# Kernel tuning notes

Hardware: AMD Instinct MI355X
Metric: run time of the kernel (lower is better)

Reference implementation:

```python
import jax, jax.numpy as jnp
import numpy as np

KERNEL, STRIDE = 3, 2
IN_DIM, OUT_DIM = 32, 32
POSE = 4
POSE_LEN = POSE * POSE
ITERS = 3
LAM = 0.01
EPS = 1e-8


def setup_inputs() -> dict:
    key = jax.random.key(0)
    k1, k2, k3, k4 = jax.random.split(key, 4)
    B, H, W = 8, 24, 24
    capsules = jax.random.uniform(k1, (B, H, W, IN_DIM, POSE_LEN + 1), dtype=jnp.float32)
    trans_mat = jax.random.normal(k2, (KERNEL, KERNEL, IN_DIM, OUT_DIM, POSE, POSE), dtype=jnp.float32)
    beta_u = jax.random.normal(k3, (1,), dtype=jnp.float32)
    beta_a = jax.random.normal(k4, (1,), dtype=jnp.float32)
    return {"capsules": capsules, "trans_mat": trans_mat, "beta_u": beta_u, "beta_a": beta_a}


def _extract_patches(capsules, h, w):
    # capsules: [B,H,W,Ci,F] -> [B,h*w,k,k,Ci,F] (strided kernel x kernel windows)
    rows = STRIDE * jnp.arange(h)[:, None] + jnp.arange(KERNEL)[None, :]  # [h,k]
    cols = STRIDE * jnp.arange(w)[:, None] + jnp.arange(KERNEL)[None, :]  # [w,k]
    p = capsules[:, rows]                # [B,h,k,W,Ci,F]
    p = p[:, :, :, cols]                 # [B,h,k,w,k,Ci,F]
    p = jnp.transpose(p, (0, 1, 3, 2, 4, 5, 6))  # [B,h,w,k,k,Ci,F]
    B = capsules.shape[0]
    return p.reshape(B, h * w, KERNEL, KERNEL, IN_DIM, p.shape[-1])


def _em_routing(V, a, beta_u, beta_a):
    # V: [B,N,I,O,P] votes, a: [B,N,I,1,1] input activations
    B, N, I, O, P = V.shape
    R = jnp.full((B, N, I, O, 1), 1.0 / O, dtype=V.dtype)
    mu = a_out = None
    for it in range(ITERS):
        # ---- M-step: weighted Gaussian statistics per output capsule ----
        Ra = R * a                                            # [B,N,I,O,1]
        sum_R = Ra.sum(axis=2, keepdims=True) + EPS           # [B,N,1,O,1]
        mu = (Ra * V).sum(axis=2, keepdims=True) / sum_R      # [B,N,1,O,P]
        sigma_sq = (Ra * (V - mu) ** 2).sum(axis=2, keepdims=True) / sum_R + EPS
        cost = (beta_u + 0.5 * jnp.log(sigma_sq)) * sum_R     # [B,N,1,O,P]
        a_out = jax.nn.sigmoid(LAM * (beta_a - cost.sum(axis=-1, keepdims=True)))  # [B,N,1,O,1]
        if it < ITERS - 1:
            # ---- E-step: posterior assignment R via Gaussian log-pdf ----
            ln_p = (-((V - mu) ** 2) / (2.0 * sigma_sq)
                    - 0.5 * jnp.log(2.0 * jnp.pi * sigma_sq)).sum(axis=-1, keepdims=True)  # [B,N,I,O,1]
            R = jax.nn.softmax(ln_p + jnp.log(a_out + EPS), axis=3)
    return mu[:, :, 0], a_out[:, :, 0, :, 0]  # [B,N,O,P], [B,N,O]


def reference(capsules, trans_mat, beta_u, beta_a):
    B, H, W = capsules.shape[:3]
    h = (H - KERNEL + 1) // STRIDE
    w = (W - KERNEL + 1) // STRIDE
    patches = _extract_patches(capsules, h, w)  # [B,N,k,k,Ci,P^2+1]
    poses = patches[..., :-1].reshape(B, h * w, KERNEL, KERNEL, IN_DIM, POSE, POSE)
    acts = patches[..., -1]                      # [B,N,k,k,Ci]
    # votes: per-(k,k,Ci,Co) pose-matrix product, vectorized over all patches
    votes = jnp.einsum('bnxyipq,xyioqr->bnxyiopr', poses, trans_mat)
    V = votes.reshape(B, h * w, KERNEL * KERNEL * IN_DIM, OUT_DIM, POSE_LEN)
    a = acts.reshape(B, h * w, KERNEL * KERNEL * IN_DIM, 1, 1)
    mu, a_out = _em_routing(V, a, beta_u, beta_a)
    out = jnp.concatenate([mu.reshape(B, h, w, OUT_DIM, POSE_LEN),
                           a_out.reshape(B, h, w, OUT_DIM, 1)], axis=-1)
    return out  # [B,h,w,out_dim,pose_len+1]
```

## Files before the change

### kernel.cpp

```cpp
#include <hip/hip_runtime.h>
#include <math.h>


namespace {

constexpr int NH   = 11;
constexpr int NI   = 288;
constexpr float LAM_   = 0.01f;
constexpr float EPS_   = 1e-8f;
constexpr float LOG2PI = 1.8378770664093453f;

typedef __attribute__((ext_vector_type(2))) float f32x2;

__device__ __forceinline__ f32x2 splat(float s) { return (f32x2){s, s}; }
__device__ __forceinline__ f32x2 vfma(f32x2 a, f32x2 b, f32x2 c) {
    return __builtin_elementwise_fma(a, b, c);
}

__device__ __forceinline__ float red32_max(float x) {
    int y;
    y = __builtin_amdgcn_update_dpp(0, __float_as_int(x), 0xB1, 0xF, 0xF, true);
    x = fmaxf(x, __int_as_float(y));
    y = __builtin_amdgcn_update_dpp(0, __float_as_int(x), 0x4E, 0xF, 0xF, true);
    x = fmaxf(x, __int_as_float(y));
    y = __builtin_amdgcn_update_dpp(0, __float_as_int(x), 0x141, 0xF, 0xF, true);
    x = fmaxf(x, __int_as_float(y));
    y = __builtin_amdgcn_update_dpp(0, __float_as_int(x), 0x140, 0xF, 0xF, true);
    x = fmaxf(x, __int_as_float(y));
    y = __builtin_amdgcn_ds_swizzle(__float_as_int(x), 0x401F);
    x = fmaxf(x, __int_as_float(y));
    return x;
}
__device__ __forceinline__ float red32_sum(float x) {
    int y;
    y = __builtin_amdgcn_update_dpp(0, __float_as_int(x), 0xB1, 0xF, 0xF, true);
    x += __int_as_float(y);
    y = __builtin_amdgcn_update_dpp(0, __float_as_int(x), 0x4E, 0xF, 0xF, true);
    x += __int_as_float(y);
    y = __builtin_amdgcn_update_dpp(0, __float_as_int(x), 0x141, 0xF, 0xF, true);
    x += __int_as_float(y);
    y = __builtin_amdgcn_update_dpp(0, __float_as_int(x), 0x140, 0xF, 0xF, true);
    x += __int_as_float(y);
    y = __builtin_amdgcn_ds_swizzle(__float_as_int(x), 0x401F);
    x += __int_as_float(y);
    return x;
}

__device__ __forceinline__ void votes_pk(const float4* __restrict__ Prow4,
                                         const f32x2 T2[4][2], f32x2 V2[4][2]) {
    float4 pr0 = Prow4[0], pr1 = Prow4[1], pr2 = Prow4[2], pr3 = Prow4[3];
#pragma unroll
    for (int h = 0; h < 2; ++h) {
        {
            f32x2 s = splat(pr0.x) * T2[0][h];
            s = vfma(splat(pr0.y), T2[1][h], s);
            s = vfma(splat(pr0.z), T2[2][h], s);
            V2[0][h] = vfma(splat(pr0.w), T2[3][h], s);
        }
        {
            f32x2 s = splat(pr1.x) * T2[0][h];
            s = vfma(splat(pr1.y), T2[1][h], s);
            s = vfma(splat(pr1.z), T2[2][h], s);
            V2[1][h] = vfma(splat(pr1.w), T2[3][h], s);
        }
        {
            f32x2 s = splat(pr2.x) * T2[0][h];
            s = vfma(splat(pr2.y), T2[1][h], s);
            s = vfma(splat(pr2.z), T2[2][h], s);
            V2[2][h] = vfma(splat(pr2.w), T2[3][h], s);
        }
        {
            f32x2 s = splat(pr3.x) * T2[0][h];
            s = vfma(splat(pr3.y), T2[1][h], s);
            s = vfma(splat(pr3.z), T2[2][h], s);
            V2[3][h] = vfma(splat(pr3.w), T2[3][h], s);
        }
    }
}

__device__ __forceinline__ void load_T2(const float4* __restrict__ tp, f32x2 T2[4][2]) {
    float4 b0 = tp[0], b1 = tp[1], b2 = tp[2], b3 = tp[3];
    T2[0][0] = (f32x2){b0.x, b0.y};  T2[0][1] = (f32x2){b0.z, b0.w};
    T2[1][0] = (f32x2){b1.x, b1.y};  T2[1][1] = (f32x2){b1.z, b1.w};
    T2[2][0] = (f32x2){b2.x, b2.y};  T2[2][1] = (f32x2){b2.z, b2.w};
    T2[3][0] = (f32x2){b3.x, b3.y};  T2[3][1] = (f32x2){b3.z, b3.w};
}

template<int BASE>
__device__ __forceinline__ float finalize_half(const f32x2* m1v, const f32x2* m2v,
        const float* __restrict__ r0, const float* __restrict__ r1,
        const float* __restrict__ r2, float S, float rs, bool last,
        float* __restrict__ mu_dst, float* __restrict__ i2s_dst)
{
    float csum = 0.f;
#pragma unroll
    for (int p = 0; p < 8; ++p) {
        constexpr int B = BASE;
        float m1k = m1v[(B + p) >> 1][(B + p) & 1];
        float m2k = m2v[(B + p) >> 1][(B + p) & 1];
        float M1f = m1k + r0[B + p] + r1[B + p] + r2[B + p];
        float M2f = m2k + r0[16 + B + p] + r1[16 + B + p] + r2[16 + B + p];
        float m  = M1f * rs;
        float sg = (M2f - 2.f * m * M1f + m * m * S) * rs + EPS_;
        csum += __logf(sg);
        mu_dst[B + p] = m;
        if (!last) i2s_dst[B + p] = __fdividef(0.5f, sg);
    }
    return csum;
}

__global__ __launch_bounds__(256, 4)
void convcaps_em_kernel(const float* __restrict__ caps,
                        const float* __restrict__ Tm,
                        const float* __restrict__ bu_p,
                        const float* __restrict__ ba_p,
                        float* __restrict__ out)
{
    __shared__ float pose_s[NI][16];
    __shared__ float act_s[NI];
    __shared__ float red_s[3][32][33];
    __shared__ float mu_s[32][18];
    __shared__ float i2s_s[32][18];
    __shared__ float C_s[32];
    __shared__ float fin_s[32][17];

    const int n  = blockIdx.x;
    const int b  = blockIdx.y;
    const int oy = n / NH;
    const int ox = n - oy * NH;
    const int t  = (int)threadIdx.x;
    const int o  = t & 31;
    const int ig = t >> 5;
    const int wv = t >> 6;
    const int ln = t & 63;
    const int hi = ln >> 5;

    for (int idx = t; idx < 9 * 544; idx += 256) {
        int cell = idx / 544;
        int j    = idx - cell * 544;
        int kx   = cell / 3;
        int ky   = cell - kx * 3;
        size_t src = ((((size_t)b * 24 + (2 * oy + kx)) * 24 + (2 * ox + ky)) * 32) * 17 + j;
        float v = caps[src];
        int ic = j / 17;
        int c  = j - ic * 17;
        int i  = cell * 32 + ic;
        if (c == 16) act_s[i] = v;
        else         pose_s[i][c] = v;
    }
    __syncthreads();

    const float beta_u = bu_p[0];
    const float beta_a = ba_p[0];
    const size_t oblk = ((((size_t)b * NH + oy) * NH + ox) * 32) * 17;

    f32x2 m1v[8], m2v[8];
    float sR;

#pragma unroll
    for (int j = 0; j < 8; ++j) { m1v[j] = splat(0.f); m2v[j] = splat(0.f); }
    sR = 0.f;
    {
        const float4* tptr = reinterpret_cast<const float4*>(Tm) + ((size_t)ig * 32 + o) * 4;
        for (int ii = 0; ii < NI / 8; ++ii, tptr += 1024) {
            const int i = ig + ii * 8;
            float ra = act_s[i] * (1.0f / 32.0f);
            f32x2 T2[4][2], V2[4][2];
            load_T2(tptr, T2);
            votes_pk(reinterpret_cast<const float4*>(&pose_s[i][0]), T2, V2);
            f32x2 ra2 = splat(ra);
#pragma unroll
            for (int p = 0; p < 4; ++p) {
#pragma unroll
                for (int h = 0; h < 2; ++h) {
                    f32x2 rv = ra2 * V2[p][h];
                    m1v[p * 2 + h] += rv;
                    m2v[p * 2 + h] = vfma(rv, V2[p][h], m2v[p * 2 + h]);
                }
            }
            sR += ra;
        }
    }

    for (int it = 0; it < 3; ++it) {
#pragma unroll
        for (int j = 0; j < 8; ++j) {
            m1v[j][0] += __shfl_xor(m1v[j][0], 32);
            m1v[j][1] += __shfl_xor(m1v[j][1], 32);
            m2v[j][0] += __shfl_xor(m2v[j][0], 32);
            m2v[j][1] += __shfl_xor(m2v[j][1], 32);
        }
        sR += __shfl_xor(sR, 32);
        if (wv > 0 && ln < 32) {
#pragma unroll
            for (int j = 0; j < 8; ++j) {
                red_s[wv - 1][o][2 * j]          = m1v[j][0];
                red_s[wv - 1][o][2 * j + 1]      = m1v[j][1];
                red_s[wv - 1][o][16 + 2 * j]     = m2v[j][0];
                red_s[wv - 1][o][16 + 2 * j + 1] = m2v[j][1];
            }
            red_s[wv - 1][o][32] = sR;
        }
        __syncthreads();

        if (wv == 0) {
            const bool last = (it == 2);
            const float* r0 = &red_s[0][o][0];
            const float* r1 = &red_s[1][o][0];
            const float* r2 = &red_s[2][o][0];
            float S    = sR + r0[32] + r1[32] + r2[32];
            float sumR = S + EPS_;
            float rs   = __fdividef(1.f, sumR);
            float* mu_dst  = last ? &fin_s[o][0] : &mu_s[o][0];
            float* i2s_dst = &i2s_s[o][0];
            float csum = (hi == 0)
                ? finalize_half<0>(m1v, m2v, r0, r1, r2, S, rs, last, mu_dst, i2s_dst)
                : finalize_half<8>(m1v, m2v, r0, r1, r2, S, rs, last, mu_dst, i2s_dst);
            csum *= 0.5f;
            float L = csum + __shfl_xor(csum, 32);
            float cost = sumR * (16.f * beta_u + L);
            float a = __fdividef(1.f, 1.f + __expf(-(LAM_ * (beta_a - cost))));
            if (hi == 0) {
                if (last) fin_s[o][16] = a;
                else      C_s[o] = __logf(a + EPS_) - (L + 8.f * LOG2PI);
            }
        }
        if (it == 2) break;
        __syncthreads();

        const float Cc = C_s[o];
        f32x2 MU2[8], IS2[8];
        {
            const f32x2* mrow = reinterpret_cast<const f32x2*>(&mu_s[o][0]);
            const f32x2* irow = reinterpret_cast<const f32x2*>(&i2s_s[o][0]);
#pragma unroll
            for (int j = 0; j < 8; ++j) { MU2[j] = mrow[j]; IS2[j] = irow[j]; }
        }

#pragma unroll
        for (int j = 0; j < 8; ++j) { m1v[j] = splat(0.f); m2v[j] = splat(0.f); }
        sR = 0.f;

        const float4* tptr = reinterpret_cast<const float4*>(Tm) + ((size_t)ig * 32 + o) * 4;
        for (int ii = 0; ii < NI / 8; ++ii, tptr += 1024) {
            const int i = ig + ii * 8;
            f32x2 T2[4][2], V2[4][2];
            load_T2(tptr, T2);
            votes_pk(reinterpret_cast<const float4*>(&pose_s[i][0]), T2, V2);

            f32x2 q2 = splat(0.f);
#pragma unroll
            for (int p = 0; p < 4; ++p) {
#pragma unroll
                for (int h = 0; h < 2; ++h) {
                    f32x2 d = V2[p][h] - MU2[p * 2 + h];
                    q2 = vfma(d * d, IS2[p * 2 + h], q2);
                }
            }
            float lnp = Cc - (q2[0] + q2[1]);

            float mx = red32_max(lnp);
            float e  = __expf(lnp - mx);
            float sm = red32_sum(e);
            float ra = __fdividef(act_s[i] * e, sm);

            f32x2 ra2 = splat(ra);
#pragma unroll
            for (int p = 0; p < 4; ++p) {
#pragma unroll
                for (int h = 0; h < 2; ++h) {
                    f32x2 rv = ra2 * V2[p][h];
                    m1v[p * 2 + h] += rv;
                    m2v[p * 2 + h] = vfma(rv, V2[p][h], m2v[p * 2 + h]);
                }
            }
            sR += ra;
        }
    }

    __syncthreads();
    for (int k = t; k < 544; k += 256) {
        out[oblk + k] = (&fin_s[0][0])[k];
    }
}

}

extern "C" void kernel_launch(void* const* d_in, const int* in_sizes, int n_in,
                              void* d_out, int out_size, void* d_ws, size_t ws_size,
                              hipStream_t stream) {
    const float* caps = (const float*)d_in[0];
    const float* Tm   = (const float*)d_in[1];
    const float* bu   = (const float*)d_in[2];
    const float* ba   = (const float*)d_in[3];
    float* out        = (float*)d_out;

    dim3 grid(121, 8);
    dim3 block(256);
    hipLaunchKernelGGL(convcaps_em_kernel, grid, block, 0, stream,
                       caps, Tm, bu, ba, out);
}
```

Baseline: 135.5 us.

## Software-pipeline E-step accumulation and drop per-input max reduction in softmax

The E-step loop is restructured so each step computes votes and the routing exponent for input i while accumulating the M-step statistics of input i-1 with double-buffered vote registers. This hides the cross-lane sum-reduction latency behind independent FMAs. The per-input max reduction is replaced by a single max of the per-output constant, which is a valid upper bound because the quadratic term is non-negative. Log-domain constants are pre-scaled by log2(e) so exp2f can be used, and the kernel is pinned to 4 waves per EU. The looser softmax shift risks underflow when the quadratic terms are large.

```diff
diff --git a/kernel.cpp b/kernel.cpp
--- a/kernel.cpp
+++ b/kernel.cpp
@@ -9,6 +9,7 @@
 constexpr float LAM_   = 0.01f;
 constexpr float EPS_   = 1e-8f;
 constexpr float LOG2PI = 1.8378770664093453f;
+constexpr float LOG2E  = 1.4426950408889634f;
 
 typedef __attribute__((ext_vector_type(2))) float f32x2;
 
@@ -46,44 +47,44 @@
     return x;
 }
 
+__device__ __forceinline__ void load_T2(const float4* __restrict__ tp, f32x2 T2[8]) {
+    float4 b0 = tp[0], b1 = tp[1], b2 = tp[2], b3 = tp[3];
+    T2[0] = (f32x2){b0.x, b0.y};  T2[1] = (f32x2){b0.z, b0.w};
+    T2[2] = (f32x2){b1.x, b1.y};  T2[3] = (f32x2){b1.z, b1.w};
+    T2[4] = (f32x2){b2.x, b2.y};  T2[5] = (f32x2){b2.z, b2.w};
+    T2[6] = (f32x2){b3.x, b3.y};  T2[7] = (f32x2){b3.z, b3.w};
+}
+
 __device__ __forceinline__ void votes_pk(const float4* __restrict__ Prow4,
-                                         const f32x2 T2[4][2], f32x2 V2[4][2]) {
+                                         const f32x2 T2[8], f32x2 V2[8]) {
     float4 pr0 = Prow4[0], pr1 = Prow4[1], pr2 = Prow4[2], pr3 = Prow4[3];
 #pragma unroll
     for (int h = 0; h < 2; ++h) {
         {
-            f32x2 s = splat(pr0.x) * T2[0][h];
-            s = vfma(splat(pr0.y), T2[1][h], s);
-            s = vfma(splat(pr0.z), T2[2][h], s);
-            V2[0][h] = vfma(splat(pr0.w), T2[3][h], s);
-        }
-        {
-            f32x2 s = splat(pr1.x) * T2[0][h];
-            s = vfma(splat(pr1.y), T2[1][h], s);
-            s = vfma(splat(pr1.z), T2[2][h], s);
-            V2[1][h] = vfma(splat(pr1.w), T2[3][h], s);
-        }
-        {
-            f32x2 s = splat(pr2.x) * T2[0][h];
-            s = vfma(splat(pr2.y), T2[1][h], s);
-            s = vfma(splat(pr2.z), T2[2][h], s);
-            V2[2][h] = vfma(splat(pr2.w), T2[3][h], s);
-        }
-        {
-            f32x2 s = splat(pr3.x) * T2[0][h];
-            s = vfma(splat(pr3.y), T2[1][h], s);
-            s = vfma(splat(pr3.z), T2[2][h], s);
-            V2[3][h] = vfma(splat(pr3.w), T2[3][h], s);
-        }
-    }
-}
-
-__device__ __forceinline__ void load_T2(const float4* __restrict__ tp, f32x2 T2[4][2]) {
-    float4 b0 = tp[0], b1 = tp[1], b2 = tp[2], b3 = tp[3];
-    T2[0][0] = (f32x2){b0.x, b0.y};  T2[0][1] = (f32x2){b0.z, b0.w};
-    T2[1][0] = (f32x2){b1.x, b1.y};  T2[1][1] = (f32x2){b1.z, b1.w};
-    T2[2][0] = (f32x2){b2.x, b2.y};  T2[2][1] = (f32x2){b2.z, b2.w};
-    T2[3][0] = (f32x2){b3.x, b3.y};  T2[3][1] = (f32x2){b3.z, b3.w};
+            f32x2 s = splat(pr0.x) * T2[h];
+            s = vfma(splat(pr0.y), T2[2 + h], s);
+            s = vfma(splat(pr0.z), T2[4 + h], s);
+            V2[h] = vfma(splat(pr0.w), T2[6 + h], s);
+        }
+        {
+            f32x2 s = splat(pr1.x) * T2[h];
+            s = vfma(splat(pr1.y), T2[2 + h], s);
+            s = vfma(splat(pr1.z), T2[4 + h], s);
+            V2[2 + h] = vfma(splat(pr1.w), T2[6 + h], s);
+        }
+        {
+            f32x2 s = splat(pr2.x) * T2[h];
+            s = vfma(splat(pr2.y), T2[2 + h], s);
+            s = vfma(splat(pr2.z), T2[4 + h], s);
+            V2[4 + h] = vfma(splat(pr2.w), T2[6 + h], s);
+        }
+        {
+            f32x2 s = splat(pr3.x) * T2[h];
+            s = vfma(splat(pr3.y), T2[2 + h], s);
+            s = vfma(splat(pr3.z), T2[4 + h], s);
+            V2[6 + h] = vfma(splat(pr3.w), T2[6 + h], s);
+        }
+    }
 }
 
 template<int BASE>
@@ -104,12 +105,46 @@
         float sg = (M2f - 2.f * m * M1f + m * m * S) * rs + EPS_;
         csum += __logf(sg);
         mu_dst[B + p] = m;
-        if (!last) i2s_dst[B + p] = __fdividef(0.5f, sg);
+        if (!last) i2s_dst[B + p] = __fdividef(0.5f, sg) * LOG2E;
     }
     return csum;
 }
 
-__global__ __launch_bounds__(256, 4)
+__device__ __forceinline__ float fused_step(
+    const float4* __restrict__ tp4, const float* __restrict__ pose_row,
+    float act, const f32x2 MU2[8], const f32x2 IS2[8], float Ccs,
+    f32x2 (&Vc)[8], const f32x2 (&Vp)[8], float raPrev,
+    f32x2 (&m1v)[8], f32x2 (&m2v)[8], float& sR)
+{
+    f32x2 T2[8];
+    load_T2(tp4, T2);
+    votes_pk(reinterpret_cast<const float4*>(pose_row), T2, Vc);
+
+    f32x2 qa = splat(0.f), qb = splat(0.f);
+#pragma unroll
+    for (int j = 0; j < 8; j += 2) {
+        f32x2 d0 = Vc[j] - MU2[j];
+        qa = vfma(d0 * d0, IS2[j], qa);
+        f32x2 d1 = Vc[j + 1] - MU2[j + 1];
+        qb = vfma(d1 * d1, IS2[j + 1], qb);
+    }
+    f32x2 q2 = qa + qb;
+    float e = exp2f(Ccs - (q2[0] + q2[1]));
+
+    f32x2 rp = splat(raPrev);
+#pragma unroll
+    for (int j = 0; j < 8; ++j) {
+        f32x2 rv = rp * Vp[j];
+        m1v[j] += rv;
+        m2v[j] = vfma(rv, Vp[j], m2v[j]);
+    }
+    sR += raPrev;
+
+    float sm = red32_sum(e);
+    return __fdividef(act * e, sm);
+}
+
+__global__ __attribute__((amdgpu_waves_per_eu(4, 4))) __launch_bounds__(256, 4)
 void convcaps_em_kernel(const float* __restrict__ caps,
                         const float* __restrict__ Tm,
                         const float* __restrict__ bu_p,
@@ -165,18 +200,15 @@
         for (int ii = 0; ii < NI / 8; ++ii, tptr += 1024) {
             const int i = ig + ii * 8;
             float ra = act_s[i] * (1.0f / 32.0f);
-            f32x2 T2[4][2], V2[4][2];
+            f32x2 T2[8], V2[8];
             load_T2(tptr, T2);
             votes_pk(reinterpret_cast<const float4*>(&pose_s[i][0]), T2, V2);
             f32x2 ra2 = splat(ra);
 #pragma unroll
-            for (int p = 0; p < 4; ++p) {
-#pragma unroll
-                for (int h = 0; h < 2; ++h) {
-                    f32x2 rv = ra2 * V2[p][h];
-                    m1v[p * 2 + h] += rv;
-                    m2v[p * 2 + h] = vfma(rv, V2[p][h], m2v[p * 2 + h]);
-                }
+            for (int j = 0; j < 8; ++j) {
+                f32x2 rv = ra2 * V2[j];
+                m1v[j] += rv;
+                m2v[j] = vfma(rv, V2[j], m2v[j]);
             }
             sR += ra;
         }
@@ -222,13 +254,14 @@
             float a = __fdividef(1.f, 1.f + __expf(-(LAM_ * (beta_a - cost))));
             if (hi == 0) {
                 if (last) fin_s[o][16] = a;
-                else      C_s[o] = __logf(a + EPS_) - (L + 8.f * LOG2PI);
+                else      C_s[o] = (__logf(a + EPS_) - (L + 8.f * LOG2PI)) * LOG2E;
             }
         }
         if (it == 2) break;
         __syncthreads();
 
-        const float Cc = C_s[o];
+        const float Cc  = C_s[o];
+        const float Ccs = Cc - red32_max(Cc);
         f32x2 MU2[8], IS2[8];
         {
             const f32x2* mrow = reinterpret_cast<const f32x2*>(&mu_s[o][0]);
@@ -241,40 +274,32 @@
         for (int j = 0; j < 8; ++j) { m1v[j] = splat(0.f); m2v[j] = splat(0.f); }
         sR = 0.f;
 
-        const float4* tptr = reinterpret_cast<const float4*>(Tm) + ((size_t)ig * 32 + o) * 4;
-        for (int ii = 0; ii < NI / 8; ++ii, tptr += 1024) {
-            const int i = ig + ii * 8;
-            f32x2 T2[4][2], V2[4][2];
-            load_T2(tptr, T2);
-            votes_pk(reinterpret_cast<const float4*>(&pose_s[i][0]), T2, V2);
-
-            f32x2 q2 = splat(0.f);
-#pragma unroll
-            for (int p = 0; p < 4; ++p) {
-#pragma unroll
-                for (int h = 0; h < 2; ++h) {
-                    f32x2 d = V2[p][h] - MU2[p * 2 + h];
-                    q2 = vfma(d * d, IS2[p * 2 + h], q2);
-                }
+        const float4* tbase = reinterpret_cast<const float4*>(Tm) + ((size_t)ig * 32 + o) * 4;
+        f32x2 VA[8], VB[8];
+#pragma unroll
+        for (int j = 0; j < 8; ++j) VB[j] = splat(0.f);
+
+        float raA = fused_step(tbase, &pose_s[ig][0], act_s[ig],
+                               MU2, IS2, Ccs, VA, VB, 0.f, m1v, m2v, sR);
+        for (int k = 0; k < 17; ++k) {
+            const int i1 = ig + (2 * k + 1) * 8;
+            const int i2 = ig + (2 * k + 2) * 8;
+            float raB = fused_step(tbase + (size_t)(2 * k + 1) * 1024, &pose_s[i1][0], act_s[i1],
+                                   MU2, IS2, Ccs, VB, VA, raA, m1v, m2v, sR);
+            raA       = fused_step(tbase + (size_t)(2 * k + 2) * 1024, &pose_s[i2][0], act_s[i2],
+                                   MU2, IS2, Ccs, VA, VB, raB, m1v, m2v, sR);
+        }
+        float raB = fused_step(tbase + (size_t)35 * 1024, &pose_s[ig + 280][0], act_s[ig + 280],
+                               MU2, IS2, Ccs, VB, VA, raA, m1v, m2v, sR);
+        {
+            f32x2 rp = splat(raB);
+#pragma unroll
+            for (int j = 0; j < 8; ++j) {
+                f32x2 rv = rp * VB[j];
+                m1v[j] += rv;
+                m2v[j] = vfma(rv, VB[j], m2v[j]);
             }
-            float lnp = Cc - (q2[0] + q2[1]);
-
-            float mx = red32_max(lnp);
-            float e  = __expf(lnp - mx);
-            float sm = red32_sum(e);
-            float ra = __fdividef(act_s[i] * e, sm);
-
-            f32x2 ra2 = splat(ra);
-#pragma unroll
-            for (int p = 0; p < 4; ++p) {
-#pragma unroll
-                for (int h = 0; h < 2; ++h) {
-                    f32x2 rv = ra2 * V2[p][h];
-                    m1v[p * 2 + h] += rv;
-                    m2v[p * 2 + h] = vfma(rv, V2[p][h], m2v[p * 2 + h]);
-                }
-            }
-            sR += ra;
+            sR += raB;
         }
     }
 
```

Result: slower. 334.4 us (+146.8%).
